# Kernel optimization log

Measured on AMD Instinct MI355X. Metric: run time of the kernel, lower is better.

## Reference

```python
import jax, jax.numpy as jnp
import numpy as np

DIM = 256
NUM_ATOMS = 1024
SPARSITY = 8
BETA = 0.25
EPS = 1e-10


def setup_inputs() -> dict:
    key = jax.random.key(0)
    k1, k2, k3, k4 = jax.random.split(key, 4)
    z_e = jax.random.normal(k1, (32, DIM, 32, 32), dtype=jnp.float32)
    dict_w = jax.random.normal(k2, (NUM_ATOMS, DIM), dtype=jnp.float32)
    rep_w = jax.random.normal(k3, (NUM_ATOMS, DIM), dtype=jnp.float32) * (1.0 / np.sqrt(DIM))
    rep_b = jnp.zeros((NUM_ATOMS,), dtype=jnp.float32)
    return {"z_e": z_e, "dict_w": dict_w, "rep_w": rep_w, "rep_b": rep_b}


def reference(z_e, dict_w, rep_w, rep_b):
    # NCHW -> NHWC, flatten to [N, D]
    ze = jnp.transpose(z_e, (0, 2, 3, 1))
    ze_shape = ze.shape
    flat = ze.reshape(-1, DIM)  # [N, D]
    n = flat.shape[0]

    # representation: Linear + softmax over atoms
    rep = jax.nn.softmax(flat @ rep_w.T + rep_b, axis=1)  # [N, K]

    # squared distances to dictionary atoms
    dists = (jnp.sum(flat ** 2, axis=1, keepdims=True)
             + jnp.sum(dict_w ** 2, axis=1)
             - 2.0 * (flat @ dict_w.T))  # [N, K]

    # top-L smallest distances
    _, idx = jax.lax.top_k(-dists, SPARSITY)  # [N, L]

    # one-hot scatter of selected atoms
    encodings = jnp.zeros((n, NUM_ATOMS), dtype=flat.dtype)
    encodings = encodings.at[jnp.arange(n)[:, None], idx].set(1.0)

    rep_sparse = encodings * rep / SPARSITY  # [N, K]
    z_dl = (rep_sparse @ dict_w).reshape(ze_shape)  # [B, H, W, D]

    e_latent_loss = jnp.mean((jax.lax.stop_gradient(z_dl) - ze) ** 2)
    loss = BETA * e_latent_loss

    # straight-through estimator
    z_st = ze + jax.lax.stop_gradient(z_dl - ze)

    avg_probs = jnp.mean(encodings, axis=0)
    avg_probs = avg_probs / jnp.sum(avg_probs)
    perplexity = jnp.exp(-jnp.sum(avg_probs * jnp.log(avg_probs + EPS)))

    return loss, jnp.transpose(z_st, (0, 3, 1, 2)), perplexity, rep_sparse
```

## Files before the change

kernel.cpp:

```cpp
#include <hip/hip_runtime.h>
#include <hip/hip_bf16.h>
#include <stdint.h>

#define NROWS   32768
#define DIMD    256
#define NATOMS  1024

typedef short  bf16x8 __attribute__((ext_vector_type(8)));
typedef float  f32x4  __attribute__((ext_vector_type(4)));

__device__ __forceinline__ unsigned short bf16rne(float f) {
    unsigned u = __float_as_uint(f);
    u = u + 0x7FFFu + ((u >> 16) & 1u);
    return (unsigned short)(u >> 16);
}
__device__ __forceinline__ float bf16f(short h) {
    return __uint_as_float(((unsigned)(unsigned short)h) << 16);
}

__global__ __launch_bounds__(256) void vq_bprep(
    const float* __restrict__ rep_w, const float* __restrict__ dict_w,
    unsigned short* __restrict__ Bs, float* __restrict__ dnorm)
{
    const int tid = threadIdx.x;
    const int atom = blockIdx.x * 32 + (tid >> 3);
    const int kc = tid & 7;
    float ss = 0.f;
#pragma unroll
    for (int m = 0; m < 2; ++m) {
        const float* src = (m ? dict_w : rep_w) + (size_t)atom * DIMD + kc * 32;
        unsigned short* dst = Bs + (size_t)m * 262144 + (size_t)kc * 32768 + atom * 32;
#pragma unroll
        for (int q = 0; q < 8; ++q) {
            float4 v = *(const float4*)&src[q * 4];
            float fv[4] = {v.x, v.y, v.z, v.w};
            unsigned short a0[4];
#pragma unroll
            for (int e = 0; e < 4; ++e) {
                if (m) ss = fmaf(fv[e], fv[e], ss);
                a0[e] = bf16rne(fv[e]);
            }
            *(ushort4*)&dst[q * 4] = make_ushort4(a0[0], a0[1], a0[2], a0[3]);
        }
    }
    ss += __shfl_down(ss, 4, 8);
    ss += __shfl_down(ss, 2, 8);
    ss += __shfl_down(ss, 1, 8);
    if (kc == 0) dnorm[atom] = ss;
}

__device__ __forceinline__ void insk(unsigned u, unsigned (&kd)[8]) {
#pragma unroll
    for (int j = 7; j >= 1; --j)
        kd[j] = min(max(u, kd[j - 1]), kd[j]);
    kd[0] = min(u, kd[0]);
}

__device__ __forceinline__ void wave_merge_k(int lane, unsigned (&kd)[8], float& se) {
#pragma unroll
    for (int half = 32; half >= 16; half >>= 1) {
        const int src = (lane + half) & 63;
        unsigned ko[8];
#pragma unroll
        for (int j = 0; j < 8; ++j) ko[j] = (unsigned)__shfl((int)kd[j], src, 64);
        const float so = __shfl(se, src, 64);
        if (lane < half) {
            se += so;
#pragma unroll
            for (int t = 0; t < 8; ++t) insk(ko[t], kd);
        }
    }
}

__global__ __launch_bounds__(256, 3) void vq_main(
    const float* __restrict__ z_e, const unsigned short* __restrict__ Bs,
    const float* __restrict__ rep_b, const float* __restrict__ dnorm,
    float* __restrict__ rep_sparse, int* __restrict__ idx_out,
    float* __restrict__ w_out)
{
    __shared__ __align__(16) float rbS[1024];
    __shared__ __align__(16) float dnS[1024];
    __shared__ __align__(16) unsigned short zSu[32][264];
    __shared__ unsigned mKu[3][32][8];
    __shared__ float mS[3][32];
    __shared__ unsigned fK[32][8];
    __shared__ float fSum[32];

    const int tid = threadIdx.x;
    const int lane = tid & 63, w = tid >> 6;
    const int c = lane & 15, lg = lane >> 4;
    const int row0 = blockIdx.x * 32;
    const int bb = row0 >> 10, hw0 = row0 & 1023;

    for (int i = tid; i < 1024; i += 256) { rbS[i] = rep_b[i]; dnS[i] = dnorm[i]; }

    const char* pL = (const char*)Bs;
    const char* pD = (const char*)Bs + 524288;
    const int abase = w << 8;

    bf16x8 bL[8], bD[8];
    {
        const int off = ((abase + c) << 6) + (lg << 4);
#pragma unroll
        for (int kc = 0; kc < 8; ++kc) {
            bL[kc] = *(const bf16x8*)(pL + ((size_t)kc << 16) + off);
            bD[kc] = *(const bf16x8*)(pD + ((size_t)kc << 16) + off);
        }
    }

    bf16x8 A0[8], A1[8];
    {
        const float* zb = z_e + (size_t)bb * 262144 + hw0 + c;
#pragma unroll
        for (int kc = 0; kc < 8; ++kc) {
            float f0[8], f1[8];
#pragma unroll
            for (int e = 0; e < 8; ++e) {
                const float* p = zb + (size_t)(kc * 32 + lg * 8 + e) * 1024;
                f0[e] = p[0];
                f1[e] = p[16];
            }
#pragma unroll
            for (int e = 0; e < 8; ++e) {
                const int k = kc * 32 + lg * 8 + e;
                const unsigned short b0 = bf16rne(f0[e]);
                const unsigned short b1 = bf16rne(f1[e]);
                zSu[c][k] = b0;
                zSu[16 + c][k] = b1;
                A0[kc][e] = (short)b0;
                A1[kc][e] = (short)b1;
            }
        }
    }
    __syncthreads();

    unsigned kd0[8], kd1[8];
    float se0 = 0.f, se1 = 0.f;
#pragma unroll
    for (int j = 0; j < 8; ++j) { kd0[j] = 0xFFFFFFFFu; kd1[j] = 0xFFFFFFFFu; }

    for (int it = 0; it < 16; ++it) {
        const int tb = abase + (it << 4) + (lg << 2);
        const f32x4 rbv = *(const f32x4*)&rbS[tb];
        const f32x4 dnv = *(const f32x4*)&dnS[tb];

        f32x4 aL0 = {0.f,0.f,0.f,0.f}, aD0 = {0.f,0.f,0.f,0.f};
        f32x4 aL1 = {0.f,0.f,0.f,0.f}, aD1 = {0.f,0.f,0.f,0.f};
#pragma unroll
        for (int kc = 0; kc < 8; ++kc) {
            aL0 = __builtin_amdgcn_mfma_f32_16x16x32_bf16(bL[kc], A0[kc], aL0, 0, 0, 0);
            aD0 = __builtin_amdgcn_mfma_f32_16x16x32_bf16(bD[kc], A0[kc], aD0, 0, 0, 0);
            aL1 = __builtin_amdgcn_mfma_f32_16x16x32_bf16(bL[kc], A1[kc], aL1, 0, 0, 0);
            aD1 = __builtin_amdgcn_mfma_f32_16x16x32_bf16(bD[kc], A1[kc], aD1, 0, 0, 0);
        }

        if (it < 15) {
            const int off = ((abase + (it + 1) * 16 + c) << 6) + (lg << 4);
#pragma unroll
            for (int kc = 0; kc < 8; ++kc) {
                bL[kc] = *(const bf16x8*)(pL + ((size_t)kc << 16) + off);
                bD[kc] = *(const bf16x8*)(pD + ((size_t)kc << 16) + off);
            }
        }

#pragma unroll
        for (int q = 0; q < 4; ++q) {
            const unsigned atom = (unsigned)(tb + q);
            se0 += __expf(aL0[q] + rbv[q]);
            se1 += __expf(aL1[q] + rbv[q]);
            unsigned u0 = __float_as_uint(dnv[q] - 2.0f * aD0[q]);
            u0 ^= ((unsigned)((int)u0 >> 31) | 0x80000000u);
            unsigned u1 = __float_as_uint(dnv[q] - 2.0f * aD1[q]);
            u1 ^= ((unsigned)((int)u1 >> 31) | 0x80000000u);
            insk((u0 & ~1023u) | atom, kd0);
            insk((u1 & ~1023u) | atom, kd1);
        }
    }

    wave_merge_k(lane, kd0, se0);
    wave_merge_k(lane, kd1, se1);

    if (w >= 1 && lane < 16) {
#pragma unroll
        for (int j = 0; j < 8; ++j) {
            mKu[w - 1][c][j] = kd0[j];
            mKu[w - 1][16 + c][j] = kd1[j];
        }
        mS[w - 1][c] = se0;
        mS[w - 1][16 + c] = se1;
    }
    __syncthreads();

    {
        float4 z4 = {0.f, 0.f, 0.f, 0.f};
        float4* rp4 = (float4*)rep_sparse + (size_t)row0 * (NATOMS / 4) + tid;
        for (int r = 0; r < 32; ++r)
            rp4[(size_t)r * (NATOMS / 4)] = z4;
    }

    if (w == 0 && lane < 16) {
        for (int p = 0; p < 3; ++p)
#pragma unroll
            for (int t = 0; t < 8; ++t) {
                insk(mKu[p][c][t], kd0);
                insk(mKu[p][16 + c][t], kd1);
            }
        se0 += mS[0][c] + mS[1][c] + mS[2][c];
        se1 += mS[0][16 + c] + mS[1][16 + c] + mS[2][16 + c];
#pragma unroll
        for (int j = 0; j < 8; ++j) { fK[c][j] = kd0[j]; fK[16 + c][j] = kd1[j]; }
        fSum[c] = se0;
        fSum[16 + c] = se1;
    }
    __syncthreads();

    {
        const int j = tid >> 5, rr = tid & 31;
        const unsigned key = fK[rr][j];
        const int idx = (int)(key & 1023u);
        float acc = 0.f;
        for (int kc = 0; kc < 8; ++kc) {
            bf16x8 rv[4], zv[4];
#pragma unroll
            for (int m = 0; m < 4; ++m) {
                rv[m] = *(const bf16x8*)(pL + ((size_t)kc << 16) + idx * 64 + m * 16);
                zv[m] = *(const bf16x8*)&zSu[rr][kc * 32 + m * 8];
            }
#pragma unroll
            for (int m = 0; m < 4; ++m)
#pragma unroll
                for (int e = 0; e < 8; ++e)
                    acc = fmaf(bf16f(zv[m][e]), bf16f(rv[m][e]), acc);
        }
        const float l = acc + rbS[idx];
        const float wv = __expf(l) * 0.125f / fSum[rr];
        const int row = row0 + rr;
        idx_out[row * 8 + j] = idx;
        w_out[row * 8 + j] = wv;
        rep_sparse[(size_t)row * NATOMS + idx] = wv;
    }
}

__global__ __launch_bounds__(256) void vq_hist(
    const int* __restrict__ idx_in, int* __restrict__ counts)
{
    __shared__ int h[1024];
    const int tid = threadIdx.x;
    for (int i = tid; i < 1024; i += 256) h[i] = 0;
    __syncthreads();
    const int4* p = (const int4*)(idx_in + blockIdx.x * 16384) + tid;
    for (int t = 0; t < 16; ++t) {
        int4 v = p[t * 256];
        atomicAdd(&h[v.x], 1); atomicAdd(&h[v.y], 1);
        atomicAdd(&h[v.z], 1); atomicAdd(&h[v.w], 1);
    }
    __syncthreads();
    for (int i = tid; i < 1024; i += 256)
        if (h[i]) atomicAdd(&counts[i], h[i]);
}

__global__ __launch_bounds__(256, 2) void vq_recon(
    const float* __restrict__ z_e, const float* __restrict__ dict_w,
    const int* __restrict__ idx_in, const float* __restrict__ w_in,
    float* __restrict__ z_st, float* __restrict__ partials)
{
    __shared__ float zdl[32][257];
    __shared__ float red[256];
    const int tid = threadIdx.x;
    const int row0 = blockIdx.x * 32;

    for (int r = 0; r < 32; ++r) {
        const int row = row0 + r;
        float acc = 0.f;
#pragma unroll
        for (int j = 0; j < 8; ++j) {
            const int ix = idx_in[row * 8 + j];
            const float wv = w_in[row * 8 + j];
            acc = fmaf(wv, dict_w[(size_t)ix * DIMD + tid], acc);
        }
        zdl[r][tid] = acc;
    }
    __syncthreads();

    const int bb = row0 >> 10, hw0 = row0 & 1023;
    const float* zb = z_e + (size_t)bb * (DIMD * 1024) + hw0;
    float* ob = z_st + (size_t)bb * (DIMD * 1024) + hw0;
    const int m = tid & 31, dg = tid >> 5;
    float sacc = 0.f;
    for (int itr = 0; itr < 32; ++itr) {
        const int d = itr * 8 + dg;
        const float ze = zb[(size_t)d * 1024 + m];
        const float zd = zdl[m][d];
        const float diff = zd - ze;
        ob[(size_t)d * 1024 + m] = ze + diff;
        sacc = fmaf(diff, diff, sacc);
    }
    red[tid] = sacc;
    __syncthreads();
    for (int s = 128; s > 0; s >>= 1) {
        if (tid < s) red[tid] += red[tid + s];
        __syncthreads();
    }
    if (tid == 0) partials[blockIdx.x] = red[0];
}

__global__ void vq_final(const float* __restrict__ partials,
                         const int* __restrict__ counts,
                         float* __restrict__ out_loss, float* __restrict__ out_perp)
{
    __shared__ double dred[256];
    __shared__ float fred[256];
    const int tid = threadIdx.x;
    double s = 0.0;
    for (int i = tid; i < 1024; i += 256) s += (double)partials[i];
    dred[tid] = s;
    __syncthreads();
    for (int st = 128; st > 0; st >>= 1) {
        if (tid < st) dred[tid] += dred[tid + st];
        __syncthreads();
    }
    float ps = 0.f;
    for (int i = tid; i < NATOMS; i += 256) {
        const float p = (float)counts[i] * (1.0f / 262144.0f);
        ps += p * logf(p + 1e-10f);
    }
    fred[tid] = ps;
    __syncthreads();
    for (int st = 128; st > 0; st >>= 1) {
        if (tid < st) fred[tid] += fred[tid + st];
        __syncthreads();
    }
    if (tid == 0) {
        *out_loss = 0.25f * (float)(dred[0] / 8388608.0);
        *out_perp = expf(-fred[0]);
    }
}

extern "C" void kernel_launch(void* const* d_in, const int* in_sizes, int n_in,
                              void* d_out, int out_size, void* d_ws, size_t ws_size,
                              hipStream_t stream) {
    const float* z_e    = (const float*)d_in[0];
    const float* dict_w = (const float*)d_in[1];
    const float* rep_w  = (const float*)d_in[2];
    const float* rep_b  = (const float*)d_in[3];

    float* out = (float*)d_out;
    float* out_loss   = out;
    float* z_st       = out + 1;
    float* out_perp   = out + 1 + 8388608;
    float* rep_sparse = out + 2 + 8388608;

    unsigned short* Bs = (unsigned short*)((((uintptr_t)(z_st + 4194304)) + 255) & ~(uintptr_t)255);

    char* ws = (char*)d_ws;
    int*   idx_out  = (int*)ws;
    float* w_out    = (float*)(ws + (1 << 20));
    int*   counts   = (int*)(ws + (2 << 20));
    float* dnorm    = (float*)(ws + (2 << 20) + 4096);
    float* partials = (float*)(ws + (2 << 20) + 8192);

    (void)hipMemsetAsync(counts, 0, NATOMS * sizeof(int), stream);

    vq_bprep<<<32, 256, 0, stream>>>(rep_w, dict_w, Bs, dnorm);
    vq_main<<<NROWS / 32, 256, 0, stream>>>(z_e, Bs, rep_b, dnorm,
                                            rep_sparse, idx_out, w_out);
    vq_hist<<<16, 256, 0, stream>>>(idx_out, counts);
    vq_recon<<<NROWS / 32, 256, 0, stream>>>(z_e, dict_w, idx_out, w_out, z_st, partials);
    vq_final<<<1, 256, 0, stream>>>(partials, counts, out_loss, out_perp);
}
```

Measured before the change: 166.9 us.

## Move selected-atom weight computation and rep_sparse writes into recon kernel

The main kernel now emits only the top-8 indices and the softmax denominators. The recon kernel zeroes rep_sparse and stages the z_e tile in shared memory once, reusing it for both the fp32 logit recompute and the residual. It then writes the weights and builds z_st from shared memory, which drops the second z_e read and the zSu staging in vq_main. It also raises recon occupancy to 4 blocks per CU. The weight logits are now computed in fp32 from rep_w instead of the bf16 copies, so they can differ slightly from the bf16 softmax denominator, and the large rep_sparse zeroing moves from vq_main into recon.

```diff
diff --git a/kernel.cpp b/kernel.cpp
--- a/kernel.cpp
+++ b/kernel.cpp
@@ -14,9 +14,6 @@
     u = u + 0x7FFFu + ((u >> 16) & 1u);
     return (unsigned short)(u >> 16);
 }
-__device__ __forceinline__ float bf16f(short h) {
-    return __uint_as_float(((unsigned)(unsigned short)h) << 16);
-}
 
 __global__ __launch_bounds__(256) void vq_bprep(
     const float* __restrict__ rep_w, const float* __restrict__ dict_w,
@@ -75,12 +72,10 @@
 __global__ __launch_bounds__(256, 3) void vq_main(
     const float* __restrict__ z_e, const unsigned short* __restrict__ Bs,
     const float* __restrict__ rep_b, const float* __restrict__ dnorm,
-    float* __restrict__ rep_sparse, int* __restrict__ idx_out,
-    float* __restrict__ w_out)
+    int* __restrict__ idx_out, float* __restrict__ fsum_out)
 {
     __shared__ __align__(16) float rbS[1024];
     __shared__ __align__(16) float dnS[1024];
-    __shared__ __align__(16) unsigned short zSu[32][264];
     __shared__ unsigned mKu[3][32][8];
     __shared__ float mS[3][32];
     __shared__ unsigned fK[32][8];
@@ -122,13 +117,8 @@
             }
 #pragma unroll
             for (int e = 0; e < 8; ++e) {
-                const int k = kc * 32 + lg * 8 + e;
-                const unsigned short b0 = bf16rne(f0[e]);
-                const unsigned short b1 = bf16rne(f1[e]);
-                zSu[c][k] = b0;
-                zSu[16 + c][k] = b1;
-                A0[kc][e] = (short)b0;
-                A1[kc][e] = (short)b1;
+                A0[kc][e] = (short)bf16rne(f0[e]);
+                A1[kc][e] = (short)bf16rne(f1[e]);
             }
         }
     }
@@ -191,13 +181,6 @@
     }
     __syncthreads();
 
-    {
-        float4 z4 = {0.f, 0.f, 0.f, 0.f};
-        float4* rp4 = (float4*)rep_sparse + (size_t)row0 * (NATOMS / 4) + tid;
-        for (int r = 0; r < 32; ++r)
-            rp4[(size_t)r * (NATOMS / 4)] = z4;
-    }
-
     if (w == 0 && lane < 16) {
         for (int p = 0; p < 3; ++p)
 #pragma unroll
@@ -216,29 +199,9 @@
 
     {
         const int j = tid >> 5, rr = tid & 31;
-        const unsigned key = fK[rr][j];
-        const int idx = (int)(key & 1023u);
-        float acc = 0.f;
-        for (int kc = 0; kc < 8; ++kc) {
-            bf16x8 rv[4], zv[4];
-#pragma unroll
-            for (int m = 0; m < 4; ++m) {
-                rv[m] = *(const bf16x8*)(pL + ((size_t)kc << 16) + idx * 64 + m * 16);
-                zv[m] = *(const bf16x8*)&zSu[rr][kc * 32 + m * 8];
-            }
-#pragma unroll
-            for (int m = 0; m < 4; ++m)
-#pragma unroll
-                for (int e = 0; e < 8; ++e)
-                    acc = fmaf(bf16f(zv[m][e]), bf16f(rv[m][e]), acc);
-        }
-        const float l = acc + rbS[idx];
-        const float wv = __expf(l) * 0.125f / fSum[rr];
-        const int row = row0 + rr;
-        idx_out[row * 8 + j] = idx;
-        w_out[row * 8 + j] = wv;
-        rep_sparse[(size_t)row * NATOMS + idx] = wv;
-    }
+        idx_out[(row0 + rr) * 8 + j] = (int)(fK[rr][j] & 1023u);
+    }
+    if (tid < 32) fsum_out[row0 + tid] = fSum[tid];
 }
 
 __global__ __launch_bounds__(256) void vq_hist(
@@ -259,42 +222,89 @@
         if (h[i]) atomicAdd(&counts[i], h[i]);
 }
 
-__global__ __launch_bounds__(256, 2) void vq_recon(
+__global__ __launch_bounds__(256, 4) void vq_recon(
     const float* __restrict__ z_e, const float* __restrict__ dict_w,
-    const int* __restrict__ idx_in, const float* __restrict__ w_in,
-    float* __restrict__ z_st, float* __restrict__ partials)
-{
-    __shared__ float zdl[32][257];
+    const float* __restrict__ rep_w, const float* __restrict__ rep_b,
+    const int* __restrict__ idx_in, const float* __restrict__ fsum_in,
+    float* __restrict__ rep_sparse, float* __restrict__ z_st,
+    float* __restrict__ partials)
+{
+    __shared__ __align__(16) float zL[32][260];
+    __shared__ int   iS[256];
+    __shared__ float wS[256];
+    __shared__ float fS[32];
     __shared__ float red[256];
+
     const int tid = threadIdx.x;
     const int row0 = blockIdx.x * 32;
-
+    const int bb = row0 >> 10, hw0 = row0 & 1023;
+    const float* zb = z_e + (size_t)bb * 262144 + hw0;
+
+    {
+        float4 z4 = {0.f, 0.f, 0.f, 0.f};
+        float4* rp4 = (float4*)rep_sparse + (size_t)row0 * (NATOMS / 4) + tid;
+        for (int r = 0; r < 32; ++r)
+            rp4[(size_t)r * (NATOMS / 4)] = z4;
+    }
+
+    iS[tid] = idx_in[row0 * 8 + tid];
+    if (tid < 32) fS[tid] = fsum_in[row0 + tid];
+    {
+        const int m = tid & 31, dg = tid >> 5;
+        for (int it = 0; it < 32; ++it) {
+            const int d = it * 8 + dg;
+            zL[m][d] = zb[(size_t)d * 1024 + m];
+        }
+    }
+    __syncthreads();
+
+    {
+        const int j = tid >> 5, rr = tid & 31;
+        const int idx = iS[rr * 8 + j];
+        const float* rw = rep_w + (size_t)idx * DIMD;
+        float acc = 0.f;
+        for (int k = 0; k < DIMD; k += 4) {
+            const float4 rv = *(const float4*)&rw[k];
+            const f32x4 zv = *(const f32x4*)&zL[rr][k];
+            acc = fmaf(zv[0], rv.x, acc);
+            acc = fmaf(zv[1], rv.y, acc);
+            acc = fmaf(zv[2], rv.z, acc);
+            acc = fmaf(zv[3], rv.w, acc);
+        }
+        wS[rr * 8 + j] = __expf(acc + rep_b[idx]) * 0.125f / fS[rr];
+    }
+    __syncthreads();
+
+    {
+        const int j = tid >> 5, rr = tid & 31;
+        rep_sparse[(size_t)(row0 + rr) * NATOMS + iS[rr * 8 + j]] = wS[rr * 8 + j];
+    }
+
+    float sacc = 0.f;
     for (int r = 0; r < 32; ++r) {
-        const int row = row0 + r;
         float acc = 0.f;
 #pragma unroll
         for (int j = 0; j < 8; ++j) {
-            const int ix = idx_in[row * 8 + j];
-            const float wv = w_in[row * 8 + j];
+            const int ix = iS[r * 8 + j];
+            const float wv = wS[r * 8 + j];
             acc = fmaf(wv, dict_w[(size_t)ix * DIMD + tid], acc);
         }
-        zdl[r][tid] = acc;
-    }
-    __syncthreads();
-
-    const int bb = row0 >> 10, hw0 = row0 & 1023;
-    const float* zb = z_e + (size_t)bb * (DIMD * 1024) + hw0;
-    float* ob = z_st + (size_t)bb * (DIMD * 1024) + hw0;
-    const int m = tid & 31, dg = tid >> 5;
-    float sacc = 0.f;
-    for (int itr = 0; itr < 32; ++itr) {
-        const int d = itr * 8 + dg;
-        const float ze = zb[(size_t)d * 1024 + m];
-        const float zd = zdl[m][d];
-        const float diff = zd - ze;
-        ob[(size_t)d * 1024 + m] = ze + diff;
+        const float ze = zL[r][tid];
+        const float diff = acc - ze;
         sacc = fmaf(diff, diff, sacc);
-    }
+        zL[r][tid] = acc;
+    }
+    __syncthreads();
+
+    {
+        float* ob = z_st + (size_t)bb * 262144 + hw0;
+        const int m = tid & 31, dg = tid >> 5;
+        for (int it = 0; it < 32; ++it) {
+            const int d = it * 8 + dg;
+            ob[(size_t)d * 1024 + m] = zL[m][d];
+        }
+    }
+
     red[tid] = sacc;
     __syncthreads();
     for (int s = 128; s > 0; s >>= 1) {
@@ -354,17 +364,19 @@
 
     char* ws = (char*)d_ws;
     int*   idx_out  = (int*)ws;
-    float* w_out    = (float*)(ws + (1 << 20));
-    int*   counts   = (int*)(ws + (2 << 20));
-    float* dnorm    = (float*)(ws + (2 << 20) + 4096);
-    float* partials = (float*)(ws + (2 << 20) + 8192);
+    float* fsum_out = (float*)(ws + (1 << 20));
+    int*   counts   = (int*)(ws + (1 << 20) + (1 << 17));
+    float* dnorm    = (float*)(ws + (1 << 20) + (1 << 17) + 4096);
+    float* partials = (float*)(ws + (1 << 20) + (1 << 17) + 8192);
 
     (void)hipMemsetAsync(counts, 0, NATOMS * sizeof(int), stream);
 
     vq_bprep<<<32, 256, 0, stream>>>(rep_w, dict_w, Bs, dnorm);
     vq_main<<<NROWS / 32, 256, 0, stream>>>(z_e, Bs, rep_b, dnorm,
-                                            rep_sparse, idx_out, w_out);
+                                            idx_out, fsum_out);
     vq_hist<<<16, 256, 0, stream>>>(idx_out, counts);
-    vq_recon<<<NROWS / 32, 256, 0, stream>>>(z_e, dict_w, idx_out, w_out, z_st, partials);
+    vq_recon<<<NROWS / 32, 256, 0, stream>>>(z_e, dict_w, rep_w, rep_b,
+                                             idx_out, fsum_out,
+                                             rep_sparse, z_st, partials);
     vq_final<<<1, 256, 0, stream>>>(partials, counts, out_loss, out_perp);
 }
```

Result: no change. 168.2 us (+0.7%).
